# Performance work log

Measured on AMD Instinct MI355X. Metric: run time of the kernel, lower is better.

Reference implementation:

```python
import jax, jax.numpy as jnp
import numpy as np

B, N, D = 4, 2048, 1024


def setup_inputs() -> dict:
    key = jax.random.key(0)
    ks = jax.random.split(key, 9)
    x = jax.random.normal(ks[0], (B, N, D), dtype=jnp.float32)
    # causal mask: True = masked (set to -inf), per dot_product_attention semantics
    mask = jnp.triu(jnp.ones((N, N), dtype=bool), k=1)
    mask = jnp.broadcast_to(mask, (B, N, N))
    scale = 1.0 / np.sqrt(D)
    Wq = jax.random.normal(ks[1], (D, D), dtype=jnp.float32) * scale
    Wk = jax.random.normal(ks[2], (D, D), dtype=jnp.float32) * scale
    Wv = jax.random.normal(ks[3], (D, D), dtype=jnp.float32) * scale
    Wo = jax.random.normal(ks[4], (D, D), dtype=jnp.float32) * scale
    bq = jnp.zeros((D,), dtype=jnp.float32)
    bk = jnp.zeros((D,), dtype=jnp.float32)
    bv = jnp.zeros((D,), dtype=jnp.float32)
    bo = jnp.zeros((D,), dtype=jnp.float32)
    return {"x": x, "mask": mask, "Wq": Wq, "bq": bq, "Wk": Wk, "bk": bk,
            "Wv": Wv, "bv": bv, "Wo": Wo, "bo": bo}


def reference(x, mask, Wq, bq, Wk, bk, Wv, bv, Wo, bo):
    # QKV projections (single-head despite docstring; module never splits heads)
    Q = x @ Wq + bq  # [b, n, d]
    K = x @ Wk + bk
    V = x @ Wv + bv
    d = K.shape[-1]
    scores = jnp.einsum('bqd,bkd->bqk', Q, K) / jnp.sqrt(jnp.asarray(d, Q.dtype))
    min_infty = jnp.finfo(scores.dtype).min
    scores = jnp.where(mask, min_infty, scores)
    weights = jax.nn.softmax(scores, axis=-1)
    attention = jnp.einsum('bqk,bkd->bqd', weights, V)
    out = attention @ Wo + bo
    return out
```

## Files before the change

### kernel.cpp

```cpp
#include <hip/hip_runtime.h>
#include <hip/hip_bf16.h>

typedef __attribute__((ext_vector_type(8))) short short8;
typedef __attribute__((ext_vector_type(4))) float f32x4;

__device__ inline float b2f(unsigned short u) {
    union { unsigned int i; float f; } c; c.i = ((unsigned int)u) << 16; return c.f;
}
__device__ inline unsigned short f2b(float f) {
    __hip_bfloat16 h = __float2bfloat16(f);
    return *reinterpret_cast<unsigned short*>(&h);
}

__device__ inline void gl_lds16(const unsigned short* g, unsigned short* ldsbase) {
    __builtin_amdgcn_global_load_lds(
        (const __attribute__((address_space(1))) unsigned int*)(g),
        (__attribute__((address_space(3))) unsigned int*)(ldsbase),
        16, 0, 0);
}

__global__ __launch_bounds__(256) void prep(
    const float* __restrict__ x,
    const float* __restrict__ Wq, const float* __restrict__ Wk,
    const float* __restrict__ Wo, const float* __restrict__ Wv,
    const float* __restrict__ bv, const float* __restrict__ bo,
    unsigned short* __restrict__ xb,
    unsigned short* __restrict__ Wqt, unsigned short* __restrict__ Wkt,
    unsigned short* __restrict__ Wot, unsigned short* __restrict__ Wvb,
    float* __restrict__ bvo)
{
    const int z = blockIdx.z;
    const int t = threadIdx.x;
    __shared__ float tile[32][33];

    if (z < 3) {
        const float* src = z == 0 ? Wq : z == 1 ? Wk : Wo;
        unsigned short* dst = z == 0 ? Wqt : z == 1 ? Wkt : Wot;
        const int c0 = blockIdx.x * 32, r0 = blockIdx.y * 32;
        const int tx = t & 31, ty = t >> 5;
        #pragma unroll
        for (int i = ty; i < 32; i += 8)
            tile[i][tx] = src[(long)(r0 + i) * 1024 + c0 + tx];
        __syncthreads();
        #pragma unroll
        for (int i = ty; i < 32; i += 8)
            dst[(long)(c0 + i) * 1024 + r0 + tx] = f2b(tile[tx][i]);
        return;
    }
    if (z == 3) {
        const int i = (blockIdx.y * 32 + blockIdx.x) * 256 + t;
        float4 v = ((const float4*)Wv)[i];
        union { unsigned short u[4]; unsigned long long ll; } p;
        p.u[0] = f2b(v.x); p.u[1] = f2b(v.y); p.u[2] = f2b(v.z); p.u[3] = f2b(v.w);
        ((unsigned long long*)Wvb)[i] = p.ll;
        return;
    }
    if (z < 6) {
        const int bl = (z - 4) * 1024 + blockIdx.y * 32 + blockIdx.x;
        #pragma unroll
        for (int k = 0; k < 4; k++) {
            const int i = bl * 1024 + k * 256 + t;
            float4 v = ((const float4*)x)[i];
            union { unsigned short u[4]; unsigned long long ll; } p;
            p.u[0] = f2b(v.x); p.u[1] = f2b(v.y); p.u[2] = f2b(v.z); p.u[3] = f2b(v.w);
            ((unsigned long long*)xb)[i] = p.ll;
        }
        return;
    }
    if (blockIdx.y != 0) return;
    const int tx = t & 31, ty = t >> 5;
    const int n = blockIdx.x * 32 + tx;
    float acc = 0.f;
    #pragma unroll 4
    for (int j = 0; j < 128; j++) {
        const int k = ty * 128 + j;
        acc += Wo[(long)k * 1024 + n] * bv[k];
    }
    float* red = &tile[0][0];
    red[ty * 32 + tx] = acc;
    __syncthreads();
    if (ty == 0) {
        float s = 0.f;
        #pragma unroll
        for (int j = 0; j < 8; j++) s += red[j * 32 + tx];
        bvo[n] = s + bo[n];
    }
}

#define TILE_KLOOP(As, Bs, gA, lda, gB, ldb, Keff) \
    for (int k0 = 0; k0 < (Keff); k0 += 64) { \
        _Pragma("unroll") for (int p = 0; p < 2; p++) \
            _Pragma("unroll") for (int h = 0; h < 2; h++) { \
                gl_lds16((gA) + (long)h * 16 * (lda) + k0 + p * 32, \
                         &(As)[p * 4096 + (w * 32 + h * 16) * 32]); \
                gl_lds16((gB) + (long)h * 16 * (ldb) + k0 + p * 32, \
                         &(Bs)[p * 4096 + (w * 32 + h * 16) * 32]); \
            } \
        __syncthreads(); \
        _Pragma("unroll") for (int p = 0; p < 2; p++) { \
            short8 af[4], bfr[4]; \
            _Pragma("unroll") for (int mi = 0; mi < 4; mi++) \
                af[mi] = *(const short8*)&(As)[p * 4096 + (wr * 64 + mi * 16 + lrow) * 32 + quad * 8]; \
            _Pragma("unroll") for (int ni = 0; ni < 4; ni++) \
                bfr[ni] = *(const short8*)&(Bs)[p * 4096 + (wc * 64 + ni * 16 + lrow) * 32 + quad * 8]; \
            _Pragma("unroll") for (int mi = 0; mi < 4; mi++) \
                _Pragma("unroll") for (int ni = 0; ni < 4; ni++) \
                    acc[mi][ni] = __builtin_amdgcn_mfma_f32_16x16x32_bf16( \
                        af[mi], bfr[ni], acc[mi][ni], 0, 0, 0); \
        } \
        __syncthreads(); \
    }

#define TILE_DECLS \
    const int t = threadIdx.x, lane = t & 63, w = t >> 6; \
    const int wr = w >> 1, wc = w & 1; \
    const int lrow = lane & 15, quad = lane >> 4; \
    f32x4 acc[4][4]; \
    _Pragma("unroll") for (int i = 0; i < 4; i++) \
        _Pragma("unroll") for (int j = 0; j < 4; j++) \
            acc[i][j] = (f32x4){0.f, 0.f, 0.f, 0.f};

template<bool TRI, bool KCAUSAL, int OMODE>
__global__ __launch_bounds__(256) void gemm128(
    const unsigned short* __restrict__ A, const unsigned short* __restrict__ Bt,
    const float* __restrict__ bias, void* __restrict__ Cv,
    int K, int lda, int ldb, int ldc, long sA, long sB, long sC, float scale)
{
    __shared__ __attribute__((aligned(16))) unsigned short As[2 * 128 * 32];
    __shared__ __attribute__((aligned(16))) unsigned short Bs[2 * 128 * 32];
    int bm, bn, bz;
    if (TRI) {
        const int q = gridDim.x - 1 - blockIdx.x;
        bm = (int)((sqrtf(8.f * q + 1.f) - 1.f) * 0.5f);
        while ((bm + 1) * (bm + 2) / 2 <= q) bm++;
        while (bm * (bm + 1) / 2 > q) bm--;
        bn = q - bm * (bm + 1) / 2;
        bz = blockIdx.y;
    } else {
        bm = KCAUSAL ? (gridDim.x - 1 - blockIdx.x) : blockIdx.x;
        bn = blockIdx.y; bz = blockIdx.z;
    }
    A  += (long)bz * sA;
    Bt += (long)bz * sB;
    const int m0 = bm * 128, n0 = bn * 128;

    TILE_DECLS

    const int Keff = KCAUSAL ? ((bm + 1) * 128 < K ? (bm + 1) * 128 : K) : K;
    const unsigned short* gA = A  + (long)(m0 + w * 32 + (lane >> 2)) * lda + (lane & 3) * 8;
    const unsigned short* gB = Bt + (long)(n0 + w * 32 + (lane >> 2)) * ldb + (lane & 3) * 8;
    TILE_KLOOP(As, Bs, gA, lda, gB, ldb, Keff)

    #pragma unroll
    for (int mi = 0; mi < 4; mi++) {
        const int m = m0 + wr * 64 + mi * 16 + quad * 4;
        #pragma unroll
        for (int ni = 0; ni < 4; ni++) {
            const int n = n0 + wc * 64 + ni * 16 + lrow;
            const float bvl = bias ? bias[n] : 0.f;
            #pragma unroll
            for (int rg = 0; rg < 4; rg++) {
                const float val = acc[mi][ni][rg] * scale + bvl;
                if (OMODE == 1)
                    ((float*)Cv)[(long)bz * sC + (long)(m + rg) * ldc + n] = val;
                else
                    ((unsigned short*)Cv)[(long)bz * sC + (long)(m + rg) * ldc + n] = f2b(val);
            }
        }
    }
}

__global__ __launch_bounds__(256) void qkv_proj(
    const unsigned short* __restrict__ A,
    const unsigned short* __restrict__ Wqt, const unsigned short* __restrict__ Wkt,
    const unsigned short* __restrict__ Wvot,
    const float* __restrict__ bq, const float* __restrict__ bk,
    unsigned short* __restrict__ Q, unsigned short* __restrict__ Km,
    unsigned short* __restrict__ Vot)
{
    __shared__ __attribute__((aligned(16))) unsigned short pool[16384];
    unsigned short* As = pool;
    unsigned short* Bs = pool + 8192;

    const int bm = blockIdx.y, bx = blockIdx.x;
    const int r = bx >> 3, bnn = bx & 7;
    const unsigned short* Bt = (r == 0) ? Wqt : (r == 1) ? Wkt : Wvot;
    const float* bias = (r == 0) ? bq : (r == 1) ? bk : nullptr;
    const int m0 = bm * 128, n0 = bnn * 128;

    TILE_DECLS

    const unsigned short* gA = A  + (long)(m0 + w * 32 + (lane >> 2)) * 1024 + (lane & 3) * 8;
    const unsigned short* gB = Bt + (long)(n0 + w * 32 + (lane >> 2)) * 1024 + (lane & 3) * 8;
    TILE_KLOOP(As, Bs, gA, 1024, gB, 1024, 1024)

    if (r < 2) {
        #pragma unroll
        for (int mi = 0; mi < 4; mi++) {
            #pragma unroll
            for (int ni = 0; ni < 4; ni++) {
                const int n_l = wc * 64 + ni * 16 + lrow;
                const float bvl = bias[n0 + n_l];
                #pragma unroll
                for (int rg = 0; rg < 4; rg++) {
                    const int m_l = wr * 64 + mi * 16 + quad * 4 + rg;
                    pool[m_l * 128 + n_l] = f2b(acc[mi][ni][rg] + bvl);
                }
            }
        }
        __syncthreads();
        unsigned short* out = (r == 0) ? Q : Km;
        #pragma unroll
        for (int it = 0; it < 8; it++) {
            const int idx = it * 256 + t;
            const int m_l = idx >> 4, c = idx & 15;
            short8 v = *(const short8*)&pool[m_l * 128 + c * 8];
            *(short8*)&out[(long)(m0 + m_l) * 1024 + n0 + c * 8] = v;
        }
    } else {
        #pragma unroll
        for (int mi = 0; mi < 4; mi++) {
            #pragma unroll
            for (int ni = 0; ni < 4; ni++) {
                const int n_l = wc * 64 + ni * 16 + lrow;
                const int mb = wr * 64 + mi * 16 + quad * 4;
                union { unsigned short u[4]; unsigned long long ll; } pk;
                #pragma unroll
                for (int rg = 0; rg < 4; rg++) pk.u[rg] = f2b(acc[mi][ni][rg]);
                *(unsigned long long*)&pool[n_l * 128 + (mb ^ ((n_l & 15) << 3))] = pk.ll;
            }
        }
        __syncthreads();
        #pragma unroll
        for (int it = 0; it < 8; it++) {
            const int idx = it * 256 + t;
            const int n_l = idx >> 4, c = idx & 15;
            short8 v = *(const short8*)&pool[n_l * 128 + ((c * 8) ^ ((n_l & 15) << 3))];
            *(short8*)&Vot[(long)(n0 + n_l) * 8192 + m0 + c * 8] = v;
        }
    }
}

__global__ __launch_bounds__(256) void softmax_causal(unsigned short* __restrict__ S)
{
    const int i = blockIdx.x;
    const int t = threadIdx.x;
    const int padded = ((i >> 7) + 1) << 7;
    const int j0 = t * 8;
    const bool active = j0 < padded;

    __shared__ float red[4];

    for (int b = 0; b < 4; b++) {
        unsigned short* base = S + ((long)b * 2048 + i) * 2048;

        float v[8];
        if (active) {
            short8 s8 = *(const short8*)(base + j0);
            #pragma unroll
            for (int jj = 0; jj < 8; jj++)
                v[jj] = (j0 + jj <= i) ? b2f((unsigned short)s8[jj]) : -3.0e38f;
        } else {
            #pragma unroll
            for (int jj = 0; jj < 8; jj++) v[jj] = -3.0e38f;
        }

        float lmax = v[0];
        #pragma unroll
        for (int jj = 1; jj < 8; jj++) lmax = fmaxf(lmax, v[jj]);
        #pragma unroll
        for (int off = 32; off > 0; off >>= 1) lmax = fmaxf(lmax, __shfl_xor(lmax, off, 64));
        if ((t & 63) == 0) red[t >> 6] = lmax;
        __syncthreads();
        const float gmax = fmaxf(fmaxf(red[0], red[1]), fmaxf(red[2], red[3]));
        __syncthreads();

        float lsum = 0.f;
        #pragma unroll
        for (int jj = 0; jj < 8; jj++) {
            v[jj] = (v[jj] > -1.0e37f) ? __expf(v[jj] - gmax) : 0.f;
            lsum += v[jj];
        }
        #pragma unroll
        for (int off = 32; off > 0; off >>= 1) lsum += __shfl_xor(lsum, off, 64);
        if ((t & 63) == 0) red[t >> 6] = lsum;
        __syncthreads();
        const float inv = 1.0f / (red[0] + red[1] + red[2] + red[3]);

        if (active) {
            short8 p8;
            #pragma unroll
            for (int jj = 0; jj < 8; jj++) p8[jj] = (short)f2b(v[jj] * inv);
            *(short8*)(base + j0) = p8;
        }
        __syncthreads();
    }
}

extern "C" void kernel_launch(void* const* d_in, const int* in_sizes, int n_in,
                              void* d_out, int out_size, void* d_ws, size_t ws_size,
                              hipStream_t stream)
{
    const float* x  = (const float*)d_in[0];
    const float* Wq = (const float*)d_in[2];
    const float* bq = (const float*)d_in[3];
    const float* Wk = (const float*)d_in[4];
    const float* bk = (const float*)d_in[5];
    const float* Wv = (const float*)d_in[6];
    const float* bv = (const float*)d_in[7];
    const float* Wo = (const float*)d_in[8];
    const float* bo = (const float*)d_in[9];

    unsigned short* ws = (unsigned short*)d_ws;
    const long XSZ = 8192L * 1024;
    const long WSZ = 1024L * 1024;
    unsigned short* xb   = ws;
    unsigned short* Wqt  = ws + XSZ;
    unsigned short* Wkt  = Wqt + WSZ;
    unsigned short* Wot  = Wkt + WSZ;
    unsigned short* Wvb  = Wot + WSZ;
    unsigned short* Wvot = Wvb + WSZ;
    unsigned short* Q    = Wvot + WSZ;
    unsigned short* Km   = Q + XSZ;
    unsigned short* Vot  = Km + XSZ;
    unsigned short* S    = Vot + XSZ;
    float*          bvo  = (float*)(S + 4L * 2048 * 2048);

    const dim3 blk(256);

    prep<<<dim3(32, 32, 7), blk, 0, stream>>>(
        x, Wq, Wk, Wo, Wv, bv, bo, xb, Wqt, Wkt, Wot, Wvb, bvo);

    gemm128<false, false, 0><<<dim3(8, 8, 1), blk, 0, stream>>>(
        Wot, Wvb, nullptr, Wvot, 1024, 1024, 1024, 1024, 0, 0, 0, 1.f);

    qkv_proj<<<dim3(24, 64), blk, 0, stream>>>(
        xb, Wqt, Wkt, Wvot, bq, bk, Q, Km, Vot);

    gemm128<true, false, 0><<<dim3(136, 4), blk, 0, stream>>>(
        Q, Km, nullptr, S, 1024, 1024, 1024, 2048,
        2048L * 1024, 2048L * 1024, 2048L * 2048, 0.03125f);

    softmax_causal<<<dim3(2048), blk, 0, stream>>>(S);

    gemm128<false, true, 1><<<dim3(16, 8, 4), blk, 0, stream>>>(
        S, Vot, bvo, (float*)d_out, 2048, 2048, 8192, 1024,
        2048L * 2048, 2048, 2048L * 1024, 1.f);
}
```

Measured before the change: 343.7 us.

## Fuse Q/K/V projection tiles so each block reuses one x tile across three weights

The QKV projection kernel now computes the Q, K and V output tiles for the same 128x128 region in a single block, loading the x tile once and multiplying it against three weight tiles held in shared memory. This cuts the redundant global reads of the activation tile, which was fetched three times before, and drops the grid from 1536 to 512 blocks. In exchange each block holds three accumulator sets (192 floats per thread) and uses 64KB of LDS, so register pressure and occupancy may get worse. The K loop is also not double-buffered.

```diff
diff --git a/kernel.cpp b/kernel.cpp
--- a/kernel.cpp
+++ b/kernel.cpp
@@ -170,7 +170,7 @@
     }
 }
 
-__global__ __launch_bounds__(256) void qkv_proj(
+__global__ __launch_bounds__(256, 2) void qkv_proj(
     const unsigned short* __restrict__ A,
     const unsigned short* __restrict__ Wqt, const unsigned short* __restrict__ Wkt,
     const unsigned short* __restrict__ Wvot,
@@ -178,66 +178,150 @@
     unsigned short* __restrict__ Q, unsigned short* __restrict__ Km,
     unsigned short* __restrict__ Vot)
 {
-    __shared__ __attribute__((aligned(16))) unsigned short pool[16384];
-    unsigned short* As = pool;
-    unsigned short* Bs = pool + 8192;
-
-    const int bm = blockIdx.y, bx = blockIdx.x;
-    const int r = bx >> 3, bnn = bx & 7;
-    const unsigned short* Bt = (r == 0) ? Wqt : (r == 1) ? Wkt : Wvot;
-    const float* bias = (r == 0) ? bq : (r == 1) ? bk : nullptr;
+    __shared__ __attribute__((aligned(16))) unsigned short smem[32768];
+    unsigned short* As  = smem;
+    unsigned short* Bs0 = smem + 8192;
+    unsigned short* Bs1 = smem + 16384;
+    unsigned short* Bs2 = smem + 24576;
+    unsigned short* pool = smem;
+
+    const int bid = blockIdx.x;
+    const int bnn = bid & 7, bm = bid >> 3;
     const int m0 = bm * 128, n0 = bnn * 128;
 
-    TILE_DECLS
-
-    const unsigned short* gA = A  + (long)(m0 + w * 32 + (lane >> 2)) * 1024 + (lane & 3) * 8;
-    const unsigned short* gB = Bt + (long)(n0 + w * 32 + (lane >> 2)) * 1024 + (lane & 3) * 8;
-    TILE_KLOOP(As, Bs, gA, 1024, gB, 1024, 1024)
-
-    if (r < 2) {
-        #pragma unroll
-        for (int mi = 0; mi < 4; mi++) {
-            #pragma unroll
-            for (int ni = 0; ni < 4; ni++) {
-                const int n_l = wc * 64 + ni * 16 + lrow;
-                const float bvl = bias[n0 + n_l];
+    const int t = threadIdx.x, lane = t & 63, w = t >> 6;
+    const int wr = w >> 1, wc = w & 1;
+    const int lrow = lane & 15, quad = lane >> 4;
+
+    f32x4 accQ[4][4], accK[4][4], accV[4][4];
+    #pragma unroll
+    for (int i = 0; i < 4; i++)
+        #pragma unroll
+        for (int j = 0; j < 4; j++) {
+            accQ[i][j] = (f32x4){0.f, 0.f, 0.f, 0.f};
+            accK[i][j] = (f32x4){0.f, 0.f, 0.f, 0.f};
+            accV[i][j] = (f32x4){0.f, 0.f, 0.f, 0.f};
+        }
+
+    const long rowA = (long)(m0 + w * 32 + (lane >> 2)) * 1024 + (lane & 3) * 8;
+    const long rowB = (long)(n0 + w * 32 + (lane >> 2)) * 1024 + (lane & 3) * 8;
+    const unsigned short* gA  = A    + rowA;
+    const unsigned short* gB0 = Wqt  + rowB;
+    const unsigned short* gB1 = Wkt  + rowB;
+    const unsigned short* gB2 = Wvot + rowB;
+
+    for (int k0 = 0; k0 < 1024; k0 += 64) {
+        #pragma unroll
+        for (int p = 0; p < 2; p++)
+            #pragma unroll
+            for (int h = 0; h < 2; h++) {
+                const int ldst = p * 4096 + (w * 32 + h * 16) * 32;
+                const long gofs = (long)h * 16 * 1024 + k0 + p * 32;
+                gl_lds16(gA  + gofs, &As[ldst]);
+                gl_lds16(gB0 + gofs, &Bs0[ldst]);
+                gl_lds16(gB1 + gofs, &Bs1[ldst]);
+                gl_lds16(gB2 + gofs, &Bs2[ldst]);
+            }
+        __syncthreads();
+        #pragma unroll
+        for (int p = 0; p < 2; p++) {
+            short8 af[4], bfr[4];
+            #pragma unroll
+            for (int mi = 0; mi < 4; mi++)
+                af[mi] = *(const short8*)&As[p * 4096 + (wr * 64 + mi * 16 + lrow) * 32 + quad * 8];
+            #pragma unroll
+            for (int ni = 0; ni < 4; ni++)
+                bfr[ni] = *(const short8*)&Bs0[p * 4096 + (wc * 64 + ni * 16 + lrow) * 32 + quad * 8];
+            #pragma unroll
+            for (int mi = 0; mi < 4; mi++)
                 #pragma unroll
-                for (int rg = 0; rg < 4; rg++) {
-                    const int m_l = wr * 64 + mi * 16 + quad * 4 + rg;
-                    pool[m_l * 128 + n_l] = f2b(acc[mi][ni][rg] + bvl);
-                }
+                for (int ni = 0; ni < 4; ni++)
+                    accQ[mi][ni] = __builtin_amdgcn_mfma_f32_16x16x32_bf16(
+                        af[mi], bfr[ni], accQ[mi][ni], 0, 0, 0);
+            #pragma unroll
+            for (int ni = 0; ni < 4; ni++)
+                bfr[ni] = *(const short8*)&Bs1[p * 4096 + (wc * 64 + ni * 16 + lrow) * 32 + quad * 8];
+            #pragma unroll
+            for (int mi = 0; mi < 4; mi++)
+                #pragma unroll
+                for (int ni = 0; ni < 4; ni++)
+                    accK[mi][ni] = __builtin_amdgcn_mfma_f32_16x16x32_bf16(
+                        af[mi], bfr[ni], accK[mi][ni], 0, 0, 0);
+            #pragma unroll
+            for (int ni = 0; ni < 4; ni++)
+                bfr[ni] = *(const short8*)&Bs2[p * 4096 + (wc * 64 + ni * 16 + lrow) * 32 + quad * 8];
+            #pragma unroll
+            for (int mi = 0; mi < 4; mi++)
+                #pragma unroll
+                for (int ni = 0; ni < 4; ni++)
+                    accV[mi][ni] = __builtin_amdgcn_mfma_f32_16x16x32_bf16(
+                        af[mi], bfr[ni], accV[mi][ni], 0, 0, 0);
+        }
+        __syncthreads();
+    }
+
+    #pragma unroll
+    for (int mi = 0; mi < 4; mi++)
+        #pragma unroll
+        for (int ni = 0; ni < 4; ni++) {
+            const int n_l = wc * 64 + ni * 16 + lrow;
+            const float bvl = bq[n0 + n_l];
+            #pragma unroll
+            for (int rg = 0; rg < 4; rg++) {
+                const int m_l = wr * 64 + mi * 16 + quad * 4 + rg;
+                pool[m_l * 128 + n_l] = f2b(accQ[mi][ni][rg] + bvl);
             }
         }
-        __syncthreads();
-        unsigned short* out = (r == 0) ? Q : Km;
-        #pragma unroll
-        for (int it = 0; it < 8; it++) {
-            const int idx = it * 256 + t;
-            const int m_l = idx >> 4, c = idx & 15;
-            short8 v = *(const short8*)&pool[m_l * 128 + c * 8];
-            *(short8*)&out[(long)(m0 + m_l) * 1024 + n0 + c * 8] = v;
-        }
-    } else {
-        #pragma unroll
-        for (int mi = 0; mi < 4; mi++) {
-            #pragma unroll
-            for (int ni = 0; ni < 4; ni++) {
-                const int n_l = wc * 64 + ni * 16 + lrow;
-                const int mb = wr * 64 + mi * 16 + quad * 4;
-                union { unsigned short u[4]; unsigned long long ll; } pk;
-                #pragma unroll
-                for (int rg = 0; rg < 4; rg++) pk.u[rg] = f2b(acc[mi][ni][rg]);
-                *(unsigned long long*)&pool[n_l * 128 + (mb ^ ((n_l & 15) << 3))] = pk.ll;
+    __syncthreads();
+    #pragma unroll
+    for (int it = 0; it < 8; it++) {
+        const int idx = it * 256 + t;
+        const int m_l = idx >> 4, c = idx & 15;
+        short8 v = *(const short8*)&pool[m_l * 128 + c * 8];
+        *(short8*)&Q[(long)(m0 + m_l) * 1024 + n0 + c * 8] = v;
+    }
+    __syncthreads();
+
+    #pragma unroll
+    for (int mi = 0; mi < 4; mi++)
+        #pragma unroll
+        for (int ni = 0; ni < 4; ni++) {
+            const int n_l = wc * 64 + ni * 16 + lrow;
+            const float bvl = bk[n0 + n_l];
+            #pragma unroll
+            for (int rg = 0; rg < 4; rg++) {
+                const int m_l = wr * 64 + mi * 16 + quad * 4 + rg;
+                pool[m_l * 128 + n_l] = f2b(accK[mi][ni][rg] + bvl);
             }
         }
-        __syncthreads();
-        #pragma unroll
-        for (int it = 0; it < 8; it++) {
-            const int idx = it * 256 + t;
-            const int n_l = idx >> 4, c = idx & 15;
-            short8 v = *(const short8*)&pool[n_l * 128 + ((c * 8) ^ ((n_l & 15) << 3))];
-            *(short8*)&Vot[(long)(n0 + n_l) * 8192 + m0 + c * 8] = v;
-        }
+    __syncthreads();
+    #pragma unroll
+    for (int it = 0; it < 8; it++) {
+        const int idx = it * 256 + t;
+        const int m_l = idx >> 4, c = idx & 15;
+        short8 v = *(const short8*)&pool[m_l * 128 + c * 8];
+        *(short8*)&Km[(long)(m0 + m_l) * 1024 + n0 + c * 8] = v;
+    }
+    __syncthreads();
+
+    #pragma unroll
+    for (int mi = 0; mi < 4; mi++)
+        #pragma unroll
+        for (int ni = 0; ni < 4; ni++) {
+            const int n_l = wc * 64 + ni * 16 + lrow;
+            const int mb = wr * 64 + mi * 16 + quad * 4;
+            union { unsigned short u[4]; unsigned long long ll; } pk;
+            #pragma unroll
+            for (int rg = 0; rg < 4; rg++) pk.u[rg] = f2b(accV[mi][ni][rg]);
+            *(unsigned long long*)&pool[n_l * 128 + (mb ^ ((n_l & 15) << 3))] = pk.ll;
+        }
+    __syncthreads();
+    #pragma unroll
+    for (int it = 0; it < 8; it++) {
+        const int idx = it * 256 + t;
+        const int n_l = idx >> 4, c = idx & 15;
+        short8 v = *(const short8*)&pool[n_l * 128 + ((c * 8) ^ ((n_l & 15) << 3))];
+        *(short8*)&Vot[(long)(n0 + n_l) * 8192 + m0 + c * 8] = v;
     }
 }
 
@@ -334,7 +418,7 @@
     gemm128<false, false, 0><<<dim3(8, 8, 1), blk, 0, stream>>>(
         Wot, Wvb, nullptr, Wvot, 1024, 1024, 1024, 1024, 0, 0, 0, 1.f);
 
-    qkv_proj<<<dim3(24, 64), blk, 0, stream>>>(
+    qkv_proj<<<dim3(512), blk, 0, stream>>>(
         xb, Wqt, Wkt, Wvot, bq, bk, Q, Km, Vot);
 
     gemm128<true, false, 0><<<dim3(136, 4), blk, 0, stream>>>(
```

Measured after the change: 334.1 us. 1.03x faster.
